# Optimization experiments

Hardware: AMD Instinct MI355X
Metric: run time of the kernel (lower is better)

Reference implementation:

```python
import jax, jax.numpy as jnp
import numpy as np

B, CIR_LEN, AUX_DIM, T, CD, DS, DCONV = 16, 16384, 14, 512, 256, 16, 4
SEG = CIR_LEN // T          # 32
DI = 2 * CD                 # d_inner = 512


def layer_norm(x, g, b, eps=1e-5):
    m = jnp.mean(x, -1, keepdims=True)
    v = jnp.var(x, -1, keepdims=True)
    return (x - m) * jax.lax.rsqrt(v + eps) * g + b


def gelu(x):
    return jax.nn.gelu(x, approximate=False)  # torch default exact GELU


def selective_ssm(x, in_proj_w, conv_w, conv_b, x_proj_w, dt_proj_w, dt_proj_b, A_log, D, out_proj_w):
    # x: (B, L, CD)
    Bsz, L, _ = x.shape
    xz = x @ in_proj_w.T                      # (B, L, 2*DI)
    x_in, z = jnp.split(xz, 2, axis=-1)       # each (B, L, DI)
    # depthwise causal conv (pad d_conv-1 left, truncate to L == torch pad both + [:L])
    xp = jnp.pad(x_in, ((0, 0), (DCONV - 1, 0), (0, 0)))
    x_conv = sum(xp[:, k:k + L, :] * conv_w[:, k] for k in range(DCONV)) + conv_b
    x_conv = jax.nn.silu(x_conv)              # (B, L, DI)
    ssm_in = x_conv @ x_proj_w.T              # (B, L, 1+2*DS)
    dt_raw = ssm_in[..., :1]
    B_ssm = ssm_in[..., 1:1 + DS]             # (B, L, DS)
    C_ssm = ssm_in[..., 1 + DS:]              # (B, L, DS)
    delta = jax.nn.softplus(dt_raw @ dt_proj_w.T + dt_proj_b)      # (B, L, DI)
    A = -jnp.exp(A_log)                                            # (DI, DS)
    deltaA = jnp.exp(delta[..., None] * A)                         # (B, L, DI, DS)
    deltaB_u = delta[..., None] * B_ssm[:, :, None, :] * x_conv[..., None]

    def step(h, inp):
        dA, dBu, c = inp
        h = dA * h + dBu                       # (B, DI, DS)
        y = jnp.einsum('bds,bs->bd', h, c)     # (B, DI)
        return h, y

    h0 = jnp.zeros((Bsz, DI, DS), x.dtype)
    _, ys = jax.lax.scan(step, h0, (jnp.moveaxis(deltaA, 1, 0),
                                    jnp.moveaxis(deltaB_u, 1, 0),
                                    jnp.moveaxis(C_ssm, 1, 0)))
    y = jnp.moveaxis(ys, 0, 1)                 # (B, L, DI)
    y = y + x_conv * D
    y = y * jax.nn.silu(z)
    return y @ out_proj_w.T                    # (B, L, CD)


def setup_inputs() -> dict:
    key = jax.random.key(0)
    ks = iter(jax.random.split(key, 32))
    rn = lambda shape, s=0.02: jax.random.normal(next(ks), shape, jnp.float32) * s
    return {
        'cir': jax.random.normal(next(ks), (B, CIR_LEN), jnp.float32),
        'aux': jax.random.normal(next(ks), (B, AUX_DIM), jnp.float32),
        'cir_proj_w': rn((CD, SEG)),
        'cir_norm_g': jnp.ones((CD,)), 'cir_norm_b': jnp.zeros((CD,)),
        'aux_proj_w': rn((CD, AUX_DIM)),
        'aux_norm_g': jnp.ones((CD,)), 'aux_norm_b': jnp.zeros((CD,)),
        'm_norm_g': jnp.ones((CD,)), 'm_norm_b': jnp.zeros((CD,)),
        'in_proj_w': rn((2 * DI, CD)),
        'conv_w': rn((DI, DCONV)), 'conv_b': jnp.zeros((DI,)),
        'x_proj_w': rn((1 + 2 * DS, DI)),
        'dt_proj_w': rn((DI, 1)), 'dt_proj_b': jnp.zeros((DI,)),
        'A_log': jnp.log(jnp.broadcast_to(jnp.arange(1, DS + 1, dtype=jnp.float32), (DI, DS))),
        'D': jnp.ones((DI,)),
        'out_proj_w': rn((CD, DI)),
        'mid_w': rn((CD, CD)), 'mid_b': jnp.zeros((CD,)),
        'mid_norm_g': jnp.ones((CD,)), 'mid_norm_b': jnp.zeros((CD,)),
        'bn_g': jnp.ones((CD,)), 'bn_b': jnp.zeros((CD,)),
        'fc1_w': rn((CD // 2, CD)), 'fc1_b': jnp.zeros((CD // 2,)),
        'fc2_w': rn((1, CD // 2)), 'fc2_b': jnp.zeros((1,)),
    }


def reference(cir, aux, cir_proj_w, cir_norm_g, cir_norm_b, aux_proj_w, aux_norm_g, aux_norm_b,
              m_norm_g, m_norm_b, in_proj_w, conv_w, conv_b, x_proj_w, dt_proj_w, dt_proj_b,
              A_log, D, out_proj_w, mid_w, mid_b, mid_norm_g, mid_norm_b, bn_g, bn_b,
              fc1_w, fc1_b, fc2_w, fc2_b):
    # eval mode: dropout = identity, BatchNorm uses running stats (mean 0, var 1)
    x_seg = cir.reshape(cir.shape[0], T, SEG)
    h_cir = gelu(layer_norm(x_seg @ cir_proj_w.T, cir_norm_g, cir_norm_b))
    h_aux = gelu(layer_norm(aux @ aux_proj_w.T, aux_norm_g, aux_norm_b))[:, None, :]
    h = h_cir + h_aux                          # (B, T, CD)
    h = h + selective_ssm(layer_norm(h, m_norm_g, m_norm_b), in_proj_w, conv_w, conv_b,
                          x_proj_w, dt_proj_w, dt_proj_b, A_log, D, out_proj_w)
    hp = jnp.mean(h, axis=1)                   # AdaptiveAvgPool1d(1)
    h2 = gelu(layer_norm(hp @ mid_w.T + mid_b, mid_norm_g, mid_norm_b))
    hbn = h2 * jax.lax.rsqrt(jnp.float32(1.0 + 1e-5)) * bn_g + bn_b
    h3 = gelu(hbn @ fc1_w.T + fc1_b)
    return (h3 @ fc2_w.T + fc2_b)[:, 0]
```

## Files before the change

kernel.cpp:

```cpp
#include <hip/hip_runtime.h>
#include <hip/hip_bf16.h>

typedef __hip_bfloat16 bf16;
typedef __attribute__((ext_vector_type(8))) short short8;
typedef __attribute__((ext_vector_type(4))) float f32x4;

#define Bsz   16
#define Tn    512
#define SEG   32
#define CD    256
#define DI    512
#define DS    16
#define DCONV 4
#define BT    (Bsz*Tn)
#define CHK   16
#define TC    32
#define NPART 32

__device__ __forceinline__ float erf_fast(float x) {
  float ax = fabsf(x);
  float t = 1.0f / (1.0f + 0.3275911f * ax);
  float p = t * (0.254829592f + t * (-0.284496736f + t * (1.421413741f +
            t * (-1.453152027f + t * 1.061405429f))));
  float r = 1.0f - p * __expf(-ax * ax);
  return copysignf(r, x);
}
__device__ __forceinline__ float gelu_f(float x) {
  return 0.5f * x * (1.0f + erf_fast(x * 0.7071067811865476f));
}
__device__ __forceinline__ float silu_f(float x) {
  return x / (1.0f + __expf(-x));
}
__device__ __forceinline__ float softplus_f(float x) {
  return fmaxf(x, 0.0f) + __logf(1.0f + __expf(-fabsf(x)));
}
__device__ __forceinline__ float bfu(unsigned short u) {
  return __uint_as_float(((unsigned int)u) << 16);
}
__device__ __forceinline__ unsigned short f2bfu(float x) {
  bf16 h = __float2bfloat16(x);
  return *(unsigned short*)&h;
}
__device__ __forceinline__ float block_sum256(float v, float* red) {
  int tid = threadIdx.x;
  #pragma unroll
  for (int off = 32; off > 0; off >>= 1) v += __shfl_down(v, off, 64);
  __syncthreads();
  if ((tid & 63) == 0) red[tid >> 6] = v;
  __syncthreads();
  return red[0] + red[1] + red[2] + red[3];
}

#define POW_TREE(ap, r)            \
  ap[0] = (r);                     \
  ap[1] = (r) * (r);               \
  ap[2] = ap[1] * (r);             \
  ap[3] = ap[1] * ap[1];           \
  ap[4] = ap[3] * (r);             \
  ap[5] = ap[3] * ap[1];           \
  ap[6] = ap[3] * ap[2];           \
  ap[7] = ap[3] * ap[3];           \
  ap[8] = ap[7] * (r);             \
  ap[9] = ap[7] * ap[1];           \
  ap[10] = ap[7] * ap[2];          \
  ap[11] = ap[7] * ap[3];          \
  ap[12] = ap[7] * ap[4];          \
  ap[13] = ap[7] * ap[5];          \
  ap[14] = ap[7] * ap[6];          \
  ap[15] = ap[7] * ap[7];

__global__ __launch_bounds__(256) void prep_kernel(
    const float* __restrict__ aux, const float* __restrict__ apw,
    const float* __restrict__ g, const float* __restrict__ bb,
    const float* __restrict__ in_w, const float* __restrict__ out_w,
    const float* __restrict__ xpw, const float* __restrict__ cpw,
    bf16* __restrict__ w_in, bf16* __restrict__ w_out, bf16* __restrict__ wpad,
    bf16* __restrict__ cpwT,
    float* __restrict__ haux, float* __restrict__ hp)
{
  __shared__ float red[4];
  int i = blockIdx.x * 256 + threadIdx.x;
  if (i < 262144) {
    int e = i & 7, lane = (i >> 3) & 63, k0 = (i >> 9) & 7, nb = i >> 12;
    int fr = lane & 15, q = lane >> 4;
    w_in[i] = __float2bfloat16(in_w[(size_t)(nb * 16 + fr) * 256 + k0 * 32 + q * 8 + e]);
  } else if (i < 393216) {
    int o = i - 262144;
    int e = o & 7, lane = (o >> 3) & 63, k0 = (o >> 9) & 15, nb = o >> 13;
    int fr = lane & 15, q = lane >> 4;
    w_out[o] = __float2bfloat16(out_w[(size_t)(nb * 16 + fr) * 512 + k0 * 32 + q * 8 + e]);
  } else {
    int o = i - 393216;
    int e = o & 7, lane = (o >> 3) & 63, k0 = (o >> 9) & 15, nb = o >> 13;
    int fr = lane & 15, q = lane >> 4;
    int row = nb * 16 + fr, k = k0 * 32 + q * 8 + e;
    float v = 0.f;
    if (row < 32)       v = xpw[(1 + row) * 512 + k];
    else if (row == 32) v = xpw[k];
    wpad[o] = __float2bfloat16(v);
  }
  if (blockIdx.x >= 528 && blockIdx.x < 560) {
    int j0 = (blockIdx.x - 528) * 256 + threadIdx.x;
    int k = j0 >> 8, j = j0 & 255;
    cpwT[j0] = __float2bfloat16(cpw[j * 32 + k]);
  }
  if (blockIdx.x < 16) {
    int b = blockIdx.x, j = threadIdx.x;
    hp[b * 256 + j] = 0.f;
    float acc = 0.f;
    #pragma unroll
    for (int k = 0; k < 14; ++k)
      acc += aux[b * 14 + k] * apw[j * 14 + k];
    float s1 = block_sum256(acc, red);
    float s2 = block_sum256(acc * acc, red);
    float mean = s1 * (1.f / 256.f);
    float var  = s2 * (1.f / 256.f) - mean * mean;
    float xn = (acc - mean) * rsqrtf(var + 1e-5f) * g[j] + bb[j];
    haux[b * 256 + j] = gelu_f(xn);
  }
}

__global__ __launch_bounds__(512) void row_inproj_kernel(
    const float* __restrict__ cir, const bf16* __restrict__ cpwT,
    const float* __restrict__ cg, const float* __restrict__ cb,
    const float* __restrict__ mg, const float* __restrict__ mb,
    const float* __restrict__ haux, const bf16* __restrict__ w_in,
    bf16* __restrict__ xzbf, float* __restrict__ hp_part)
{
  __shared__ float hps[8][256];
  __shared__ __align__(16) unsigned short xns[16][264];
  int tid = threadIdx.x;
  int wave = tid >> 6, lane = tid & 63;
  int r0 = blockIdx.x * 16 + wave * 2;
  int b = blockIdx.x >> 5;
  int j0 = lane * 4;

  float vj[2][4] = {};
  for (int c = 0; c < 8; ++c) {
    float xk[2][4];
    #pragma unroll
    for (int r4 = 0; r4 < 2; ++r4) {
      float4 xv = ((const float4*)(cir + (size_t)(r0 + r4) * SEG))[c];
      xk[r4][0] = xv.x; xk[r4][1] = xv.y; xk[r4][2] = xv.z; xk[r4][3] = xv.w;
    }
    #pragma unroll
    for (int kk = 0; kk < 4; ++kk) {
      int k = c * 4 + kk;
      uint2 wv = *(const uint2*)((const unsigned short*)cpwT + k * 256 + j0);
      float w0 = __uint_as_float(wv.x << 16);
      float w1 = __uint_as_float(wv.x & 0xffff0000u);
      float w2 = __uint_as_float(wv.y << 16);
      float w3 = __uint_as_float(wv.y & 0xffff0000u);
      #pragma unroll
      for (int r4 = 0; r4 < 2; ++r4) {
        float xv = xk[r4][kk];
        vj[r4][0] += xv * w0; vj[r4][1] += xv * w1;
        vj[r4][2] += xv * w2; vj[r4][3] += xv * w3;
      }
    }
  }
  float s[2], q2[2];
  #pragma unroll
  for (int r4 = 0; r4 < 2; ++r4) {
    s[r4]  = vj[r4][0] + vj[r4][1] + vj[r4][2] + vj[r4][3];
    q2[r4] = vj[r4][0]*vj[r4][0] + vj[r4][1]*vj[r4][1]
           + vj[r4][2]*vj[r4][2] + vj[r4][3]*vj[r4][3];
  }
  #pragma unroll
  for (int off = 32; off > 0; off >>= 1) {
    #pragma unroll
    for (int r4 = 0; r4 < 2; ++r4) {
      s[r4]  += __shfl_xor(s[r4],  off, 64);
      q2[r4] += __shfl_xor(q2[r4], off, 64);
    }
  }
  float4 cgv = *(const float4*)(cg + j0);
  float4 cbv = *(const float4*)(cb + j0);
  float4 hxv = *(const float4*)(haux + b * 256 + j0);
  float hv[2][4];
  float hs[2], hq[2];
  #pragma unroll
  for (int r4 = 0; r4 < 2; ++r4) {
    float mean = s[r4] * (1.f/256.f);
    float var  = q2[r4] * (1.f/256.f) - mean * mean;
    float inv  = rsqrtf(var + 1e-5f);
    float g0 = gelu_f((vj[r4][0] - mean) * inv * cgv.x + cbv.x) + hxv.x;
    float g1 = gelu_f((vj[r4][1] - mean) * inv * cgv.y + cbv.y) + hxv.y;
    float g2 = gelu_f((vj[r4][2] - mean) * inv * cgv.z + cbv.z) + hxv.z;
    float g3 = gelu_f((vj[r4][3] - mean) * inv * cgv.w + cbv.w) + hxv.w;
    hv[r4][0] = g0; hv[r4][1] = g1; hv[r4][2] = g2; hv[r4][3] = g3;
    hs[r4] = g0 + g1 + g2 + g3;
    hq[r4] = g0*g0 + g1*g1 + g2*g2 + g3*g3;
  }
  #pragma unroll
  for (int off = 32; off > 0; off >>= 1) {
    #pragma unroll
    for (int r4 = 0; r4 < 2; ++r4) {
      hs[r4] += __shfl_xor(hs[r4], off, 64);
      hq[r4] += __shfl_xor(hq[r4], off, 64);
    }
  }
  float4 mgv = *(const float4*)(mg + j0);
  float4 mbv = *(const float4*)(mb + j0);
  #pragma unroll
  for (int r4 = 0; r4 < 2; ++r4) {
    float m2  = hs[r4] * (1.f/256.f);
    float v2  = hq[r4] * (1.f/256.f) - m2 * m2;
    float inv2 = rsqrtf(v2 + 1e-5f);
    unsigned int lo = (unsigned int)f2bfu((hv[r4][0] - m2) * inv2 * mgv.x + mbv.x) |
                      ((unsigned int)f2bfu((hv[r4][1] - m2) * inv2 * mgv.y + mbv.y) << 16);
    unsigned int hi = (unsigned int)f2bfu((hv[r4][2] - m2) * inv2 * mgv.z + mbv.z) |
                      ((unsigned int)f2bfu((hv[r4][3] - m2) * inv2 * mgv.w + mbv.w) << 16);
    uint2 pk; pk.x = lo; pk.y = hi;
    *(uint2*)&xns[wave * 2 + r4][j0] = pk;
  }
  #pragma unroll
  for (int q = 0; q < 4; ++q)
    hps[wave][j0 + q] = hv[0][q] + hv[1][q];
  __syncthreads();
  if (tid < 256) {
    int j = tid;
    float part = hps[0][j] + hps[1][j] + hps[2][j] + hps[3][j]
               + hps[4][j] + hps[5][j] + hps[6][j] + hps[7][j];
    hp_part[(size_t)(blockIdx.x & (NPART - 1)) * 4096 + b * 256 + j] =
        part * (1.f / 512.f);
  }
  {
    int fr = lane & 15, quad = lane >> 4;
    int rbase = blockIdx.x * 16;
    const short* Wp = (const short*)w_in;
    unsigned short* xzp = (unsigned short*)xzbf;
    #pragma unroll
    for (int nt = 0; nt < 8; ++nt) {
      int nb = wave * 8 + nt;
      f32x4 acc = {0.f, 0.f, 0.f, 0.f};
      #pragma unroll
      for (int k0 = 0; k0 < 8; ++k0) {
        int ka = k0 * 32 + quad * 8;
        short8 a = *(const short8*)&xns[fr][ka];
        short8 bb8 = *(const short8*)(Wp + (((size_t)nb * 8 + k0) * 64 + lane) * 8);
        acc = __builtin_amdgcn_mfma_f32_16x16x32_bf16(a, bb8, acc, 0, 0, 0);
      }
      int crow = quad * 4, n0 = nb * 16;
      #pragma unroll
      for (int i = 0; i < 4; ++i)
        xzp[(size_t)(rbase + crow + i) * 1024 + n0 + fr] = f2bfu(acc[i]);
    }
  }
}

__global__ __launch_bounds__(512) void conv_ssm1_kernel(
    const bf16* __restrict__ xzbf, const bf16* __restrict__ wpad,
    const float* __restrict__ cw, const float* __restrict__ cbv,
    const float* __restrict__ dtw, const float* __restrict__ dtb,
    bf16* __restrict__ xcbf, float* __restrict__ ssm,
    float* __restrict__ hF, float* __restrict__ Ssum)
{
  __shared__ __align__(16) unsigned short xcs[32][520];
  __shared__ float ssms[32][68];
  int c = blockIdx.x, b = blockIdx.y;
  int t0 = c * TC;
  int tid = threadIdx.x;
  const unsigned short* xzp = (const unsigned short*)xzbf;

  {
    int d = tid;
    float4 w = *(const float4*)(cw + d * 4);
    float cbd = cbv[d];
    float pa = 0.f, pb = 0.f, pc = 0.f;
    #pragma unroll
    for (int i = 0; i < 3; ++i) {
      int t = t0 - 3 + i;
      float v = (t >= 0) ? bfu(xzp[((size_t)((b << 9) + t)) * 1024 + d]) : 0.f;
      if (i == 0) pa = v; else if (i == 1) pb = v; else pc = v;
    }
    unsigned short* xco = (unsigned short*)xcbf;
    for (int i = 0; i < TC; ++i) {
      int t = t0 + i;
      float x = bfu(xzp[((size_t)((b << 9) + t)) * 1024 + d]);
      float a = cbd + w.x * pa + w.y * pb + w.z * pc + w.w * x;
      pa = pb; pb = pc; pc = x;
      unsigned short o = f2bfu(silu_f(a));
      xcs[i][d] = o;
      xco[((size_t)((b << 9) + t)) * 512 + d] = o;
    }
  }
  __syncthreads();

  {
    int wave = tid >> 6, lane = tid & 63;
    int fr = lane & 15, quad = lane >> 4;
    int mh = wave >> 2;
    int nb = wave & 3;
    int n0 = nb * 16;
    f32x4 acc = {0.f, 0.f, 0.f, 0.f};
    const short* Wp = (const short*)wpad;
    #pragma unroll
    for (int k0 = 0; k0 < 16; ++k0) {
      int ka = k0 * 32 + quad * 8;
      short8 a = *(const short8*)&xcs[mh * 16 + fr][ka];
      short8 b8 = *(const short8*)(Wp + (((size_t)nb * 16 + k0) * 64 + lane) * 8);
      acc = __builtin_amdgcn_mfma_f32_16x16x32_bf16(a, b8, acc, 0, 0, 0);
    }
    int ccol = lane & 15, crow = quad * 4;
    #pragma unroll
    for (int i = 0; i < 4; ++i) {
      ssms[mh * 16 + crow + i][n0 + ccol] = acc[i];
      ssm[((size_t)((b << 9) + t0 + mh * 16 + crow + i)) * 64 + n0 + ccol] = acc[i];
    }
  }
  __syncthreads();

  {
    int d = tid;
    float wd = dtw[d], bd = dtb[d];
    float h[16];
    #pragma unroll
    for (int s = 0; s < 16; ++s) h[s] = 0.f;
    float ss = 0.f;
    for (int i = 0; i < TC; ++i) {
      float dtraw = ssms[i][32];
      float de = softplus_f(dtraw * wd + bd);
      ss += de;
      float x = bfu(xcs[i][d]);
      float c0 = de * x;
      float r = __expf(-de);
      float ap[16];
      POW_TREE(ap, r)
      #pragma unroll
      for (int s = 0; s < 16; ++s)
        h[s] = ap[s] * h[s] + c0 * ssms[i][s];
    }
    size_t base = ((size_t)((b * CHK + c) * 512 + d)) * 16;
    float4* o = (float4*)(hF + base);
    #pragma unroll
    for (int q = 0; q < 4; ++q)
      o[q] = make_float4(h[4*q], h[4*q+1], h[4*q+2], h[4*q+3]);
    Ssum[(size_t)(b * CHK + c) * 512 + d] = ss;
  }
}

__global__ __launch_bounds__(256) void scan_combine(
    const float* __restrict__ hF, const float* __restrict__ Ssum,
    const float* __restrict__ A_log, float* __restrict__ h0)
{
  int dblk = blockIdx.x, b = blockIdx.y;
  int s = threadIdx.x & 15, dl = threadIdx.x >> 4;
  int d = dblk * 16 + dl;
  float A = -__expf(A_log[d * 16 + s]);
  float carry = 0.f;
  for (int c = 0; c < CHK; ++c) {
    size_t idx = ((size_t)((b * CHK + c) * 512 + d)) * 16 + s;
    h0[idx] = carry;
    float P = __expf(A * Ssum[(size_t)(b * CHK + c) * 512 + d]);
    carry = P * carry + hF[idx];
  }
}

__global__ __launch_bounds__(512) void ssm2_outproj_kernel(
    const float* __restrict__ ssm, const bf16* __restrict__ xcbf,
    const bf16* __restrict__ xzbf, const float* __restrict__ h0,
    const float* __restrict__ dtw, const float* __restrict__ dtb,
    const float* __restrict__ Dd, const bf16* __restrict__ w_out,
    float* __restrict__ hp)
{
  __shared__ __align__(16) unsigned short ys[32][520];
  __shared__ float ssms[32][68];
  int c = blockIdx.x, b = blockIdx.y;
  int t0 = c * TC;
  int tid = threadIdx.x;

  {
    const float4* src = (const float4*)(ssm + ((size_t)((b << 9) + t0)) * 64);
    float4 v = src[tid];
    int row = tid >> 4, col = (tid & 15) * 4;
    ssms[row][col] = v.x; ssms[row][col+1] = v.y;
    ssms[row][col+2] = v.z; ssms[row][col+3] = v.w;
  }
  __syncthreads();

  {
    int d = tid;
    float wd = dtw[d], bd = dtb[d], Dv = Dd[d];
    float h[16];
    size_t hbase = ((size_t)((b * CHK + c) * 512 + d)) * 16;
    #pragma unroll
    for (int q = 0; q < 4; ++q) {
      float4 v = ((const float4*)(h0 + hbase))[q];
      h[4*q] = v.x; h[4*q+1] = v.y; h[4*q+2] = v.z; h[4*q+3] = v.w;
    }
    const unsigned short* xcp = (const unsigned short*)xcbf;
    const unsigned short* xzp = (const unsigned short*)xzbf;
    for (int i = 0; i < TC; ++i) {
      int t = t0 + i;
      float dtraw = ssms[i][32];
      float de = softplus_f(dtraw * wd + bd);
      float x = bfu(xcp[((size_t)((b << 9) + t)) * 512 + d]);
      float z = bfu(xzp[((size_t)((b << 9) + t)) * 1024 + 512 + d]);
      float c0 = de * x;
      float r = __expf(-de);
      float ap[16];
      POW_TREE(ap, r)
      float yp0 = 0.f, yp1 = 0.f, yp2 = 0.f, yp3 = 0.f;
      #pragma unroll
      for (int s = 0; s < 16; ++s) {
        h[s] = ap[s] * h[s] + c0 * ssms[i][s];
        float term = h[s] * ssms[i][16 + s];
        if ((s & 3) == 0)      yp0 += term;
        else if ((s & 3) == 1) yp1 += term;
        else if ((s & 3) == 2) yp2 += term;
        else                   yp3 += term;
      }
      float y = (yp0 + yp1) + (yp2 + yp3);
      y = (y + x * Dv) * silu_f(z);
      ys[i][d] = f2bfu(y);
    }
  }
  __syncthreads();

  {
    int wave = tid >> 6, lane = tid & 63;
    int fr = lane & 15, quad = lane >> 4;
    const short* Wp = (const short*)w_out;
    #pragma unroll
    for (int nt2 = 0; nt2 < 2; ++nt2) {
      int nb = wave * 2 + nt2;
      int n0 = nb * 16;
      f32x4 acc0 = {0.f,0.f,0.f,0.f}, acc1 = acc0;
      #pragma unroll
      for (int k0 = 0; k0 < 16; ++k0) {
        int ka = k0 * 32 + quad * 8;
        short8 a0 = *(const short8*)&ys[fr][ka];
        short8 a1 = *(const short8*)&ys[16 + fr][ka];
        short8 b8 = *(const short8*)(Wp + (((size_t)nb * 16 + k0) * 64 + lane) * 8);
        acc0 = __builtin_amdgcn_mfma_f32_16x16x32_bf16(a0, b8, acc0, 0, 0, 0);
        acc1 = __builtin_amdgcn_mfma_f32_16x16x32_bf16(a1, b8, acc1, 0, 0, 0);
      }
      float s = acc0[0] + acc0[1] + acc0[2] + acc0[3]
              + acc1[0] + acc1[1] + acc1[2] + acc1[3];
      s += __shfl_xor(s, 16, 64);
      s += __shfl_xor(s, 32, 64);
      if (quad == 0)
        atomicAdd(&hp[b * 256 + n0 + (lane & 15)], s * (1.f / 512.f));
    }
  }
}

__global__ __launch_bounds__(256) void head_kernel(
    const float* __restrict__ hp, const float* __restrict__ hp_part,
    const float* __restrict__ midw, const float* __restrict__ midb,
    const float* __restrict__ mng, const float* __restrict__ mnb,
    const float* __restrict__ bng, const float* __restrict__ bnb,
    const float* __restrict__ f1w, const float* __restrict__ f1b,
    const float* __restrict__ f2w, const float* __restrict__ f2b,
    float* __restrict__ out)
{
  __shared__ float red[4];
  __shared__ __align__(16) float shp[256];
  __shared__ __align__(16) float sh[256];
  __shared__ __align__(16) float sh2[128];
  int b = blockIdx.x, j = threadIdx.x;
  float hv = hp[b * 256 + j];
  #pragma unroll
  for (int p = 0; p < NPART; ++p)
    hv += hp_part[(size_t)p * 4096 + b * 256 + j];
  shp[j] = hv;
  __syncthreads();
  float acc = midb[j];
  {
    const float4* mw = (const float4*)(midw + j * 256);
    const float4* sv = (const float4*)shp;
    #pragma unroll 4
    for (int k = 0; k < 64; ++k) {
      float4 w = mw[k], xv = sv[k];
      acc += w.x * xv.x + w.y * xv.y + w.z * xv.z + w.w * xv.w;
    }
  }
  float s1 = block_sum256(acc, red);
  float s2 = block_sum256(acc * acc, red);
  float mean = s1 * (1.f / 256.f);
  float var  = s2 * (1.f / 256.f) - mean * mean;
  float h2 = gelu_f((acc - mean) * rsqrtf(var + 1e-5f) * mng[j] + mnb[j]);
  float hbn = h2 * rsqrtf(1.0f + 1e-5f) * bng[j] + bnb[j];
  sh[j] = hbn;
  __syncthreads();
  if (j < 128) {
    float a2 = f1b[j];
    const float4* fw = (const float4*)(f1w + j * 256);
    const float4* sv = (const float4*)sh;
    #pragma unroll 4
    for (int k = 0; k < 64; ++k) {
      float4 w = fw[k], xv = sv[k];
      a2 += w.x * xv.x + w.y * xv.y + w.z * xv.z + w.w * xv.w;
    }
    sh2[j] = gelu_f(a2);
  }
  __syncthreads();
  if (j == 0) {
    float o = f2b[0];
    const float4* fw = (const float4*)f2w;
    const float4* sv = (const float4*)sh2;
    for (int k = 0; k < 32; ++k) {
      float4 w = fw[k], xv = sv[k];
      o += w.x * xv.x + w.y * xv.y + w.z * xv.z + w.w * xv.w;
    }
    out[b] = o;
  }
}

extern "C" void kernel_launch(void* const* d_in, const int* in_sizes, int n_in,
                              void* d_out, int out_size, void* d_ws, size_t ws_size,
                              hipStream_t stream)
{
  const float* cir        = (const float*)d_in[0];
  const float* aux        = (const float*)d_in[1];
  const float* cir_proj_w = (const float*)d_in[2];
  const float* cir_norm_g = (const float*)d_in[3];
  const float* cir_norm_b = (const float*)d_in[4];
  const float* aux_proj_w = (const float*)d_in[5];
  const float* aux_norm_g = (const float*)d_in[6];
  const float* aux_norm_b = (const float*)d_in[7];
  const float* m_norm_g   = (const float*)d_in[8];
  const float* m_norm_b   = (const float*)d_in[9];
  const float* in_proj_w  = (const float*)d_in[10];
  const float* conv_w     = (const float*)d_in[11];
  const float* conv_b     = (const float*)d_in[12];
  const float* x_proj_w   = (const float*)d_in[13];
  const float* dt_proj_w  = (const float*)d_in[14];
  const float* dt_proj_b  = (const float*)d_in[15];
  const float* A_log      = (const float*)d_in[16];
  const float* Dd         = (const float*)d_in[17];
  const float* out_proj_w = (const float*)d_in[18];
  const float* mid_w      = (const float*)d_in[19];
  const float* mid_b      = (const float*)d_in[20];
  const float* mid_norm_g = (const float*)d_in[21];
  const float* mid_norm_b = (const float*)d_in[22];
  const float* bn_g       = (const float*)d_in[23];
  const float* bn_b       = (const float*)d_in[24];
  const float* fc1_w      = (const float*)d_in[25];
  const float* fc1_b      = (const float*)d_in[26];
  const float* fc2_w      = (const float*)d_in[27];
  const float* fc2_b      = (const float*)d_in[28];
  float* out = (float*)d_out;

  float* ws    = (float*)d_ws;
  bf16*  xzbf  = (bf16*)ws;
  bf16*  xcbf  = (bf16*)(ws + 4194304);
  float* ssm   = ws + 4194304 + 2097152;
  float* hF    = ssm + 524288;
  float* h0    = hF + 2097152;
  float* Ssum  = h0 + 2097152;
  bf16*  w_inbf  = (bf16*)(Ssum + 131072);
  bf16*  w_outbf = (bf16*)((float*)w_inbf + 131072);
  bf16*  wpadbf  = (bf16*)((float*)w_outbf + 65536);
  bf16*  cpwTbf  = (bf16*)((float*)wpadbf + 16384);
  float* haux  = (float*)cpwTbf + 4096;
  float* hp    = haux + 4096;
  float* hp_part = hp + 4096;

  prep_kernel<<<1664, 256, 0, stream>>>(aux, aux_proj_w, aux_norm_g, aux_norm_b,
                                        in_proj_w, out_proj_w, x_proj_w, cir_proj_w,
                                        w_inbf, w_outbf, wpadbf, cpwTbf, haux, hp);
  row_inproj_kernel<<<512, 512, 0, stream>>>(cir, cpwTbf, cir_norm_g, cir_norm_b,
                                             m_norm_g, m_norm_b, haux, w_inbf,
                                             xzbf, hp_part);
  conv_ssm1_kernel<<<dim3(CHK, Bsz), 512, 0, stream>>>(xzbf, wpadbf, conv_w, conv_b,
                                                       dt_proj_w, dt_proj_b,
                                                       xcbf, ssm, hF, Ssum);
  scan_combine<<<dim3(32, Bsz), 256, 0, stream>>>(hF, Ssum, A_log, h0);
  ssm2_outproj_kernel<<<dim3(CHK, Bsz), 512, 0, stream>>>(ssm, xcbf, xzbf, h0,
                                                          dt_proj_w, dt_proj_b, Dd,
                                                          w_outbf, hp);
  head_kernel<<<16, 256, 0, stream>>>(hp, hp_part, mid_w, mid_b, mid_norm_g, mid_norm_b,
                                      bn_g, bn_b, fc1_w, fc1_b, fc2_w, fc2_b, out);
}
```

Before: 199.7 us.

## Replace chunked SSM scan with per-(d,s) full scan and fold out_proj into head

The chunked two-pass scan (local chunk scan, carry combine, second scan plus a per-chunk out_proj MFMA with atomics) becomes one sequential scan kernel. In it each thread owns one (d,s) state over all 512 timesteps and accumulates the time-sum of y directly. Because mean pooling is linear, out_proj is applied once to the pooled y in the head kernel, and the bf16 conversion of out_proj weights is dropped. This removes the hF/h0/xc intermediate traffic, the combine kernel and the large out_proj GEMM. In exchange the scan is a long serial dependency over 512 steps, run on only 256 blocks.

```diff
diff --git a/kernel.cpp b/kernel.cpp
--- a/kernel.cpp
+++ b/kernel.cpp
@@ -13,8 +13,6 @@
 #define DS    16
 #define DCONV 4
 #define BT    (Bsz*Tn)
-#define CHK   16
-#define TC    32
 #define NPART 32
 
 __device__ __forceinline__ float erf_fast(float x) {
@@ -51,32 +49,13 @@
   return red[0] + red[1] + red[2] + red[3];
 }
 
-#define POW_TREE(ap, r)            \
-  ap[0] = (r);                     \
-  ap[1] = (r) * (r);               \
-  ap[2] = ap[1] * (r);             \
-  ap[3] = ap[1] * ap[1];           \
-  ap[4] = ap[3] * (r);             \
-  ap[5] = ap[3] * ap[1];           \
-  ap[6] = ap[3] * ap[2];           \
-  ap[7] = ap[3] * ap[3];           \
-  ap[8] = ap[7] * (r);             \
-  ap[9] = ap[7] * ap[1];           \
-  ap[10] = ap[7] * ap[2];          \
-  ap[11] = ap[7] * ap[3];          \
-  ap[12] = ap[7] * ap[4];          \
-  ap[13] = ap[7] * ap[5];          \
-  ap[14] = ap[7] * ap[6];          \
-  ap[15] = ap[7] * ap[7];
-
 __global__ __launch_bounds__(256) void prep_kernel(
     const float* __restrict__ aux, const float* __restrict__ apw,
     const float* __restrict__ g, const float* __restrict__ bb,
-    const float* __restrict__ in_w, const float* __restrict__ out_w,
-    const float* __restrict__ xpw, const float* __restrict__ cpw,
-    bf16* __restrict__ w_in, bf16* __restrict__ w_out, bf16* __restrict__ wpad,
-    bf16* __restrict__ cpwT,
-    float* __restrict__ haux, float* __restrict__ hp)
+    const float* __restrict__ in_w, const float* __restrict__ xpw,
+    const float* __restrict__ cpw,
+    bf16* __restrict__ w_in, bf16* __restrict__ wpad, bf16* __restrict__ cpwT,
+    float* __restrict__ haux)
 {
   __shared__ float red[4];
   int i = blockIdx.x * 256 + threadIdx.x;
@@ -84,13 +63,8 @@
     int e = i & 7, lane = (i >> 3) & 63, k0 = (i >> 9) & 7, nb = i >> 12;
     int fr = lane & 15, q = lane >> 4;
     w_in[i] = __float2bfloat16(in_w[(size_t)(nb * 16 + fr) * 256 + k0 * 32 + q * 8 + e]);
-  } else if (i < 393216) {
+  } else if (i < 294912) {
     int o = i - 262144;
-    int e = o & 7, lane = (o >> 3) & 63, k0 = (o >> 9) & 15, nb = o >> 13;
-    int fr = lane & 15, q = lane >> 4;
-    w_out[o] = __float2bfloat16(out_w[(size_t)(nb * 16 + fr) * 512 + k0 * 32 + q * 8 + e]);
-  } else {
-    int o = i - 393216;
     int e = o & 7, lane = (o >> 3) & 63, k0 = (o >> 9) & 15, nb = o >> 13;
     int fr = lane & 15, q = lane >> 4;
     int row = nb * 16 + fr, k = k0 * 32 + q * 8 + e;
@@ -98,15 +72,13 @@
     if (row < 32)       v = xpw[(1 + row) * 512 + k];
     else if (row == 32) v = xpw[k];
     wpad[o] = __float2bfloat16(v);
-  }
-  if (blockIdx.x >= 528 && blockIdx.x < 560) {
-    int j0 = (blockIdx.x - 528) * 256 + threadIdx.x;
-    int k = j0 >> 8, j = j0 & 255;
-    cpwT[j0] = __float2bfloat16(cpw[j * 32 + k]);
+  } else {
+    int o = i - 294912;
+    int k = o >> 8, j = o & 255;
+    cpwT[o] = __float2bfloat16(cpw[j * 32 + k]);
   }
   if (blockIdx.x < 16) {
     int b = blockIdx.x, j = threadIdx.x;
-    hp[b * 256 + j] = 0.f;
     float acc = 0.f;
     #pragma unroll
     for (int k = 0; k < 14; ++k)
@@ -241,7 +213,8 @@
         short8 bb8 = *(const short8*)(Wp + (((size_t)nb * 8 + k0) * 64 + lane) * 8);
         acc = __builtin_amdgcn_mfma_f32_16x16x32_bf16(a, bb8, acc, 0, 0, 0);
       }
-      int crow = quad * 4, n0 = nb * 16;
+      int n0 = nb * 16;
+      int crow = quad * 4;
       #pragma unroll
       for (int i = 0; i < 4; ++i)
         xzp[(size_t)(rbase + crow + i) * 1024 + n0 + fr] = f2bfu(acc[i]);
@@ -249,17 +222,14 @@
   }
 }
 
-__global__ __launch_bounds__(512) void conv_ssm1_kernel(
+__global__ __launch_bounds__(512) void conv_xproj_kernel(
     const bf16* __restrict__ xzbf, const bf16* __restrict__ wpad,
     const float* __restrict__ cw, const float* __restrict__ cbv,
-    const float* __restrict__ dtw, const float* __restrict__ dtb,
-    bf16* __restrict__ xcbf, float* __restrict__ ssm,
-    float* __restrict__ hF, float* __restrict__ Ssum)
+    float* __restrict__ ssm)
 {
   __shared__ __align__(16) unsigned short xcs[32][520];
-  __shared__ float ssms[32][68];
   int c = blockIdx.x, b = blockIdx.y;
-  int t0 = c * TC;
+  int t0 = c * 32;
   int tid = threadIdx.x;
   const unsigned short* xzp = (const unsigned short*)xzbf;
 
@@ -274,15 +244,12 @@
       float v = (t >= 0) ? bfu(xzp[((size_t)((b << 9) + t)) * 1024 + d]) : 0.f;
       if (i == 0) pa = v; else if (i == 1) pb = v; else pc = v;
     }
-    unsigned short* xco = (unsigned short*)xcbf;
-    for (int i = 0; i < TC; ++i) {
+    for (int i = 0; i < 32; ++i) {
       int t = t0 + i;
       float x = bfu(xzp[((size_t)((b << 9) + t)) * 1024 + d]);
       float a = cbd + w.x * pa + w.y * pb + w.z * pc + w.w * x;
       pa = pb; pb = pc; pc = x;
-      unsigned short o = f2bfu(silu_f(a));
-      xcs[i][d] = o;
-      xco[((size_t)((b << 9) + t)) * 512 + d] = o;
+      xcs[i][d] = f2bfu(silu_f(a));
     }
   }
   __syncthreads();
@@ -304,150 +271,107 @@
     }
     int ccol = lane & 15, crow = quad * 4;
     #pragma unroll
-    for (int i = 0; i < 4; ++i) {
-      ssms[mh * 16 + crow + i][n0 + ccol] = acc[i];
+    for (int i = 0; i < 4; ++i)
       ssm[((size_t)((b << 9) + t0 + mh * 16 + crow + i)) * 64 + n0 + ccol] = acc[i];
-    }
-  }
-  __syncthreads();
-
-  {
-    int d = tid;
-    float wd = dtw[d], bd = dtb[d];
-    float h[16];
-    #pragma unroll
-    for (int s = 0; s < 16; ++s) h[s] = 0.f;
-    float ss = 0.f;
-    for (int i = 0; i < TC; ++i) {
-      float dtraw = ssms[i][32];
-      float de = softplus_f(dtraw * wd + bd);
-      ss += de;
-      float x = bfu(xcs[i][d]);
-      float c0 = de * x;
-      float r = __expf(-de);
-      float ap[16];
-      POW_TREE(ap, r)
-      #pragma unroll
-      for (int s = 0; s < 16; ++s)
-        h[s] = ap[s] * h[s] + c0 * ssms[i][s];
-    }
-    size_t base = ((size_t)((b * CHK + c) * 512 + d)) * 16;
-    float4* o = (float4*)(hF + base);
-    #pragma unroll
-    for (int q = 0; q < 4; ++q)
-      o[q] = make_float4(h[4*q], h[4*q+1], h[4*q+2], h[4*q+3]);
-    Ssum[(size_t)(b * CHK + c) * 512 + d] = ss;
-  }
-}
-
-__global__ __launch_bounds__(256) void scan_combine(
-    const float* __restrict__ hF, const float* __restrict__ Ssum,
-    const float* __restrict__ A_log, float* __restrict__ h0)
+  }
+}
+
+__global__ __launch_bounds__(512) void scan_full_kernel(
+    const bf16* __restrict__ xzbf, const float* __restrict__ ssm,
+    const float* __restrict__ cw, const float* __restrict__ cbv,
+    const float* __restrict__ dtw, const float* __restrict__ dtb,
+    const float* __restrict__ A_log, const float* __restrict__ Dd,
+    float* __restrict__ ybar)
 {
-  int dblk = blockIdx.x, b = blockIdx.y;
-  int s = threadIdx.x & 15, dl = threadIdx.x >> 4;
-  int d = dblk * 16 + dl;
-  float A = -__expf(A_log[d * 16 + s]);
-  float carry = 0.f;
-  for (int c = 0; c < CHK; ++c) {
-    size_t idx = ((size_t)((b * CHK + c) * 512 + d)) * 16 + s;
-    h0[idx] = carry;
-    float P = __expf(A * Ssum[(size_t)(b * CHK + c) * 512 + d]);
-    carry = P * carry + hF[idx];
-  }
-}
-
-__global__ __launch_bounds__(512) void ssm2_outproj_kernel(
-    const float* __restrict__ ssm, const bf16* __restrict__ xcbf,
-    const bf16* __restrict__ xzbf, const float* __restrict__ h0,
-    const float* __restrict__ dtw, const float* __restrict__ dtb,
-    const float* __restrict__ Dd, const bf16* __restrict__ w_out,
-    float* __restrict__ hp)
-{
-  __shared__ __align__(16) unsigned short ys[32][520];
-  __shared__ float ssms[32][68];
-  int c = blockIdx.x, b = blockIdx.y;
-  int t0 = c * TC;
+  __shared__ __align__(16) unsigned short xraw[67][32];
+  __shared__ __align__(8)  float BC[64][34];
+  __shared__ float dts[64];
+  __shared__ __align__(8)  float xcg[64][32][2];
+
+  int dgrp = blockIdx.x, b = blockIdx.y;
   int tid = threadIdx.x;
-
-  {
-    const float4* src = (const float4*)(ssm + ((size_t)((b << 9) + t0)) * 64);
-    float4 v = src[tid];
-    int row = tid >> 4, col = (tid & 15) * 4;
-    ssms[row][col] = v.x; ssms[row][col+1] = v.y;
-    ssms[row][col+2] = v.z; ssms[row][col+3] = v.w;
-  }
-  __syncthreads();
-
-  {
-    int d = tid;
-    float wd = dtw[d], bd = dtb[d], Dv = Dd[d];
-    float h[16];
-    size_t hbase = ((size_t)((b * CHK + c) * 512 + d)) * 16;
-    #pragma unroll
-    for (int q = 0; q < 4; ++q) {
-      float4 v = ((const float4*)(h0 + hbase))[q];
-      h[4*q] = v.x; h[4*q+1] = v.y; h[4*q+2] = v.z; h[4*q+3] = v.w;
-    }
-    const unsigned short* xcp = (const unsigned short*)xcbf;
-    const unsigned short* xzp = (const unsigned short*)xzbf;
-    for (int i = 0; i < TC; ++i) {
-      int t = t0 + i;
-      float dtraw = ssms[i][32];
-      float de = softplus_f(dtraw * wd + bd);
-      float x = bfu(xcp[((size_t)((b << 9) + t)) * 512 + d]);
-      float z = bfu(xzp[((size_t)((b << 9) + t)) * 1024 + 512 + d]);
-      float c0 = de * x;
-      float r = __expf(-de);
-      float ap[16];
-      POW_TREE(ap, r)
-      float yp0 = 0.f, yp1 = 0.f, yp2 = 0.f, yp3 = 0.f;
-      #pragma unroll
-      for (int s = 0; s < 16; ++s) {
-        h[s] = ap[s] * h[s] + c0 * ssms[i][s];
-        float term = h[s] * ssms[i][16 + s];
-        if ((s & 3) == 0)      yp0 += term;
-        else if ((s & 3) == 1) yp1 += term;
-        else if ((s & 3) == 2) yp2 += term;
-        else                   yp3 += term;
+  int d0 = dgrp * 32;
+  int bb = b << 9;
+  const unsigned short* xzp = (const unsigned short*)xzbf;
+
+  int s  = tid & 15;
+  int dp = tid >> 4;
+  int dS = d0 + dp;
+  float wdS = dtw[dS], bdS = dtb[dS];
+  float As  = -__expf(A_log[dS * 16 + s]);
+  int d2 = tid & 31;
+  int dC = d0 + d2;
+  float4 wc = *(const float4*)(cw + dC * 4);
+  float cbd = cbv[dC];
+
+  float h = 0.f, yacc = 0.f, xdacc = 0.f;
+
+  for (int tile = 0; tile < 8; ++tile) {
+    int t0 = tile * 64;
+    __syncthreads();
+    if (tid < 268) {
+      int row = tid >> 2, c4 = tid & 3;
+      int t = t0 - 3 + row;
+      uint4 v = make_uint4(0u, 0u, 0u, 0u);
+      if (t >= 0)
+        v = *(const uint4*)(xzp + ((size_t)(bb + t)) * 1024 + d0 + c4 * 8);
+      *(uint4*)&xraw[row][c4 * 8] = v;
+    }
+    {
+      int r = tid >> 3, l8 = tid & 7;
+      const float* srow = ssm + ((size_t)(bb + t0 + r)) * 64;
+      float4 v = *(const float4*)(srow + l8 * 4);
+      int cc = l8 * 4;
+      if (cc < 16) {
+        BC[r][cc*2]   = v.x; BC[r][cc*2+2] = v.y;
+        BC[r][cc*2+4] = v.z; BC[r][cc*2+6] = v.w;
+      } else {
+        int c2 = cc - 16;
+        BC[r][c2*2+1] = v.x; BC[r][c2*2+3] = v.y;
+        BC[r][c2*2+5] = v.z; BC[r][c2*2+7] = v.w;
       }
-      float y = (yp0 + yp1) + (yp2 + yp3);
-      y = (y + x * Dv) * silu_f(z);
-      ys[i][d] = f2bfu(y);
-    }
-  }
-  __syncthreads();
-
-  {
-    int wave = tid >> 6, lane = tid & 63;
-    int fr = lane & 15, quad = lane >> 4;
-    const short* Wp = (const short*)w_out;
-    #pragma unroll
-    for (int nt2 = 0; nt2 < 2; ++nt2) {
-      int nb = wave * 2 + nt2;
-      int n0 = nb * 16;
-      f32x4 acc0 = {0.f,0.f,0.f,0.f}, acc1 = acc0;
-      #pragma unroll
-      for (int k0 = 0; k0 < 16; ++k0) {
-        int ka = k0 * 32 + quad * 8;
-        short8 a0 = *(const short8*)&ys[fr][ka];
-        short8 a1 = *(const short8*)&ys[16 + fr][ka];
-        short8 b8 = *(const short8*)(Wp + (((size_t)nb * 16 + k0) * 64 + lane) * 8);
-        acc0 = __builtin_amdgcn_mfma_f32_16x16x32_bf16(a0, b8, acc0, 0, 0, 0);
-        acc1 = __builtin_amdgcn_mfma_f32_16x16x32_bf16(a1, b8, acc1, 0, 0, 0);
-      }
-      float s = acc0[0] + acc0[1] + acc0[2] + acc0[3]
-              + acc1[0] + acc1[1] + acc1[2] + acc1[3];
-      s += __shfl_xor(s, 16, 64);
-      s += __shfl_xor(s, 32, 64);
-      if (quad == 0)
-        atomicAdd(&hp[b * 256 + n0 + (lane & 15)], s * (1.f / 512.f));
-    }
-  }
+      if (l8 == 0) dts[r] = srow[32];
+    }
+    float zr[4];
+    #pragma unroll
+    for (int jj = 0; jj < 4; ++jj) {
+      int ii = jj * 16 + (tid >> 5);
+      zr[jj] = bfu(xzp[((size_t)(bb + t0 + ii)) * 1024 + 512 + dC]);
+    }
+    __syncthreads();
+    #pragma unroll
+    for (int jj = 0; jj < 4; ++jj) {
+      int ii = jj * 16 + (tid >> 5);
+      float xa = bfu(xraw[ii][d2]);
+      float xb = bfu(xraw[ii + 1][d2]);
+      float xm = bfu(xraw[ii + 2][d2]);
+      float xd = bfu(xraw[ii + 3][d2]);
+      float a = cbd + wc.x * xa + wc.y * xb + wc.z * xm + wc.w * xd;
+      xcg[ii][d2][0] = bfu(f2bfu(silu_f(a)));
+      xcg[ii][d2][1] = silu_f(zr[jj]);
+    }
+    __syncthreads();
+    for (int i = 0; i < 64; ++i) {
+      float de = softplus_f(dts[i] * wdS + bdS);
+      float2 xg = *(const float2*)&xcg[i][dp][0];
+      float2 bc = *(const float2*)&BC[i][s * 2];
+      float a = __expf(As * de);
+      h = a * h + (de * xg.x) * bc.x;
+      yacc  += h * bc.y * xg.y;
+      xdacc += xg.x * xg.y;
+    }
+  }
+  yacc += __shfl_xor(yacc, 1, 64);
+  yacc += __shfl_xor(yacc, 2, 64);
+  yacc += __shfl_xor(yacc, 4, 64);
+  yacc += __shfl_xor(yacc, 8, 64);
+  if (s == 0)
+    ybar[b * 512 + dS] = yacc + Dd[dS] * xdacc;
 }
 
 __global__ __launch_bounds__(256) void head_kernel(
-    const float* __restrict__ hp, const float* __restrict__ hp_part,
+    const float* __restrict__ hp_part, const float* __restrict__ ybar,
+    const float* __restrict__ w_out,
     const float* __restrict__ midw, const float* __restrict__ midb,
     const float* __restrict__ mng, const float* __restrict__ mnb,
     const float* __restrict__ bng, const float* __restrict__ bnb,
@@ -456,14 +380,29 @@
     float* __restrict__ out)
 {
   __shared__ float red[4];
+  __shared__ __align__(16) float yb[512];
   __shared__ __align__(16) float shp[256];
   __shared__ __align__(16) float sh[256];
   __shared__ __align__(16) float sh2[128];
   int b = blockIdx.x, j = threadIdx.x;
-  float hv = hp[b * 256 + j];
+  yb[j]       = ybar[b * 512 + j];
+  yb[256 + j] = ybar[b * 512 + 256 + j];
+  float hv = 0.f;
   #pragma unroll
   for (int p = 0; p < NPART; ++p)
     hv += hp_part[(size_t)p * 4096 + b * 256 + j];
+  __syncthreads();
+  {
+    float acc2 = 0.f;
+    const float4* wr = (const float4*)(w_out + j * 512);
+    const float4* yv = (const float4*)yb;
+    #pragma unroll 4
+    for (int k = 0; k < 128; ++k) {
+      float4 w = wr[k], x = yv[k];
+      acc2 += w.x * x.x + w.y * x.y + w.z * x.z + w.w * x.w;
+    }
+    hv += acc2 * (1.f / 512.f);
+  }
   shp[j] = hv;
   __syncthreads();
   float acc = midb[j];
@@ -543,34 +482,28 @@
   const float* fc2_b      = (const float*)d_in[28];
   float* out = (float*)d_out;
 
-  float* ws    = (float*)d_ws;
-  bf16*  xzbf  = (bf16*)ws;
-  bf16*  xcbf  = (bf16*)(ws + 4194304);
-  float* ssm   = ws + 4194304 + 2097152;
-  float* hF    = ssm + 524288;
-  float* h0    = hF + 2097152;
-  float* Ssum  = h0 + 2097152;
-  bf16*  w_inbf  = (bf16*)(Ssum + 131072);
-  bf16*  w_outbf = (bf16*)((float*)w_inbf + 131072);
-  bf16*  wpadbf  = (bf16*)((float*)w_outbf + 65536);
+  float* ws      = (float*)d_ws;
+  bf16*  xzbf    = (bf16*)ws;
+  float* ssm     = ws + 4194304;
+  bf16*  w_inbf  = (bf16*)(ssm + 524288);
+  bf16*  wpadbf  = (bf16*)((float*)w_inbf + 131072);
   bf16*  cpwTbf  = (bf16*)((float*)wpadbf + 16384);
-  float* haux  = (float*)cpwTbf + 4096;
-  float* hp    = haux + 4096;
-  float* hp_part = hp + 4096;
-
-  prep_kernel<<<1664, 256, 0, stream>>>(aux, aux_proj_w, aux_norm_g, aux_norm_b,
-                                        in_proj_w, out_proj_w, x_proj_w, cir_proj_w,
-                                        w_inbf, w_outbf, wpadbf, cpwTbf, haux, hp);
+  float* haux    = (float*)cpwTbf + 4096;
+  float* hp_part = haux + 4096;
+  float* ybar    = hp_part + 131072;
+
+  prep_kernel<<<1184, 256, 0, stream>>>(aux, aux_proj_w, aux_norm_g, aux_norm_b,
+                                        in_proj_w, x_proj_w, cir_proj_w,
+                                        w_inbf, wpadbf, cpwTbf, haux);
   row_inproj_kernel<<<512, 512, 0, stream>>>(cir, cpwTbf, cir_norm_g, cir_norm_b,
                                              m_norm_g, m_norm_b, haux, w_inbf,
                                              xzbf, hp_part);
-  conv_ssm1_kernel<<<dim3(CHK, Bsz), 512, 0, stream>>>(xzbf, wpadbf, conv_w, conv_b,
-                                                       dt_proj_w, dt_proj_b,
-                                                       xcbf, ssm, hF, Ssum);
-  scan_combine<<<dim3(32, Bsz), 256, 0, stream>>>(hF, Ssum, A_log, h0);
-  ssm2_outproj_kernel<<<dim3(CHK, Bsz), 512, 0, stream>>>(ssm, xcbf, xzbf, h0,
-                                                          dt_proj_w, dt_proj_b, Dd,
-                                                          w_outbf, hp);
-  head_kernel<<<16, 256, 0, stream>>>(hp, hp_part, mid_w, mid_b, mid_norm_g, mid_norm_b,
+  conv_xproj_kernel<<<dim3(16, Bsz), 512, 0, stream>>>(xzbf, wpadbf, conv_w, conv_b,
+                                                       ssm);
+  scan_full_kernel<<<dim3(16, Bsz), 512, 0, stream>>>(xzbf, ssm, conv_w, conv_b,
+                                                      dt_proj_w, dt_proj_b,
+                                                      A_log, Dd, ybar);
+  head_kernel<<<16, 256, 0, stream>>>(hp_part, ybar, out_proj_w,
+                                      mid_w, mid_b, mid_norm_g, mid_norm_b,
                                       bn_g, bn_b, fc1_w, fc1_b, fc2_w, fc2_b, out);
 }
```

Result: slower. 252.2 us (+26.3%).
